# Kernel optimization log

Measured on AMD Instinct MI355X. Metric: run time of the kernel, lower is better.

Reference implementation:

```python
import jax, jax.numpy as jnp
import numpy as np

B, S, D = 2, 2048, 1024
H = 16
HD = D // H
MLP = 4096
EPS_LN = 1e-6
EPS_NORM = 1e-12
LOG_MAX = float(np.log(1.0 / 0.01))  # clamp cap for logit_scale


def setup_inputs() -> dict:
    key = jax.random.key(0)
    ks = jax.random.split(key, 12)
    sd = 0.02
    return {
        "x": jax.random.normal(ks[0], (B, S, D), jnp.float32),
        "wq": jax.random.normal(ks[1], (D, D), jnp.float32) * sd,
        "bq": jnp.zeros((D,), jnp.float32),
        "wk": jax.random.normal(ks[2], (D, D), jnp.float32) * sd,
        "bk": jnp.zeros((D,), jnp.float32),
        "wv": jax.random.normal(ks[3], (D, D), jnp.float32) * sd,
        "bv": jnp.zeros((D,), jnp.float32),
        "wo": jax.random.normal(ks[4], (D, D), jnp.float32) * sd,
        "bo": jnp.zeros((D,), jnp.float32),
        "w1": jax.random.normal(ks[5], (D, MLP), jnp.float32) * sd,
        "b1": jax.random.normal(ks[6], (MLP,), jnp.float32) * 1e-6,
        "w2": jax.random.normal(ks[7], (MLP, D), jnp.float32) * sd,
        "b2": jax.random.normal(ks[8], (D,), jnp.float32) * 1e-6,
        "ln1_g": jnp.ones((D,), jnp.float32),
        "ln1_b": jnp.zeros((D,), jnp.float32),
        "ln2_g": jnp.ones((D,), jnp.float32),
        "ln2_b": jnp.zeros((D,), jnp.float32),
        "logit_scale": jnp.log(10.0 * jnp.ones((H, 1, 1), jnp.float32)),
    }


def _layernorm(x, g, b):
    mu = jnp.mean(x, axis=-1, keepdims=True)
    var = jnp.var(x, axis=-1, keepdims=True)
    return (x - mu) * jax.lax.rsqrt(var + EPS_LN) * g + b


def _l2norm(x):
    n = jnp.linalg.norm(x, axis=-1, keepdims=True)
    return x / jnp.maximum(n, EPS_NORM)


def _split_heads(t):  # [B,S,D] -> [B,H,S,HD]
    return t.reshape(B, S, H, HD).transpose(0, 2, 1, 3)


def reference(x, wq, bq, wk, bk, wv, bv, wo, bo, w1, b1, w2, b2,
              ln1_g, ln1_b, ln2_g, ln2_b, logit_scale):
    h = x
    xn = _layernorm(x, ln1_g, ln1_b)
    q = _split_heads(xn @ wq + bq)
    k = _split_heads(xn @ wk + bk)
    v = _split_heads(xn @ wv + bv)
    # cosine attention: L2-normalize q,k, scale by clamped learnable exp temp
    scores = jnp.einsum("bhqd,bhkd->bhqk", _l2norm(q), _l2norm(k))
    scale = jnp.exp(jnp.minimum(logit_scale, LOG_MAX))  # [H,1,1]
    scores = scores * scale
    probs = jax.nn.softmax(scores, axis=-1)
    ctx = jnp.einsum("bhqk,bhkd->bhqd", probs, v)
    ctx = ctx.transpose(0, 2, 1, 3).reshape(B, S, D)
    x = ctx @ wo + bo + h
    h = x
    xn = _layernorm(x, ln2_g, ln2_b)
    y = jax.nn.gelu(xn @ w1 + b1, approximate=False) @ w2 + b2
    return y + h
```

## Files before the change

kernel.cpp:

```cpp
#include <hip/hip_runtime.h>
#include <hip/hip_bf16.h>
#include <math.h>

typedef unsigned short u16;
typedef unsigned int u32;
typedef __attribute__((ext_vector_type(8))) short bf16x8;
typedef __attribute__((ext_vector_type(4))) float f32x4;
typedef __attribute__((ext_vector_type(16))) float f32x16;

#define S_LEN 2048
#define DM 1024
#define NH 16
#define HD 64
#define MLPD 4096
#define BSZ 2
#define NROWS (BSZ * S_LEN)
#define LOGMAX 4.60517018598809f

__device__ __forceinline__ u16 f2bf(float f) {
  u32 u = __float_as_uint(f);
  u32 r = (u + 0x7fffu + ((u >> 16) & 1u)) >> 16;
  return (u16)r;
}
__device__ __forceinline__ float bf2f(u16 h) { return __uint_as_float(((u32)h) << 16); }
__device__ __forceinline__ u32 pk2(float a, float b) {
  return (u32)f2bf(a) | ((u32)f2bf(b) << 16);
}
__device__ __forceinline__ u32 cvtpk(float a, float b) {
  u32 r;
  asm("v_cvt_pk_bf16_f32 %0, %1, %2" : "=v"(r) : "v"(a), "v"(b));
  return r;
}
__device__ __forceinline__ void gld16(const void* g, void* l) {
  __builtin_amdgcn_global_load_lds(
      (const __attribute__((address_space(1))) void*)g,
      (__attribute__((address_space(3))) void*)l, 16, 0, 0);
}

__global__ __launch_bounds__(256) void ln_bf16(const float* __restrict__ x,
                                               const float* __restrict__ g,
                                               const float* __restrict__ b,
                                               u16* __restrict__ out) {
  const int row = blockIdx.x;
  const int t = threadIdx.x;
  const float* xr = x + (size_t)row * DM;
  float4 v = *reinterpret_cast<const float4*>(xr + t * 4);
  float s = v.x + v.y + v.z + v.w;
  float s2 = v.x * v.x + v.y * v.y + v.z * v.z + v.w * v.w;
#pragma unroll
  for (int off = 32; off > 0; off >>= 1) {
    s += __shfl_down(s, off);
    s2 += __shfl_down(s2, off);
  }
  __shared__ float red[8];
  __shared__ float mv[2];
  const int wid = t >> 6, lane = t & 63;
  if (lane == 0) { red[wid] = s; red[wid + 4] = s2; }
  __syncthreads();
  if (t == 0) {
    float ts = red[0] + red[1] + red[2] + red[3];
    float ts2 = red[4] + red[5] + red[6] + red[7];
    float mu = ts * (1.0f / DM);
    float var = ts2 * (1.0f / DM) - mu * mu;
    mv[0] = mu;
    mv[1] = rsqrtf(var + 1e-6f);
  }
  __syncthreads();
  const float mu = mv[0], rs = mv[1];
  float4 gv = *reinterpret_cast<const float4*>(g + t * 4);
  float4 bv = *reinterpret_cast<const float4*>(b + t * 4);
  float o0 = (v.x - mu) * rs * gv.x + bv.x;
  float o1 = (v.y - mu) * rs * gv.y + bv.y;
  float o2 = (v.z - mu) * rs * gv.z + bv.z;
  float o3 = (v.w - mu) * rs * gv.w + bv.w;
  uint2 o;
  o.x = pk2(o0, o1);
  o.y = pk2(o2, o3);
  *reinterpret_cast<uint2*>(out + (size_t)row * DM + t * 4) = o;
}

__global__ __launch_bounds__(256) void prep_weights(
    const float* __restrict__ wq, const float* __restrict__ wk, const float* __restrict__ wv,
    const float* __restrict__ wo, const float* __restrict__ w1, const float* __restrict__ w2,
    const float* __restrict__ bq, const float* __restrict__ bk, const float* __restrict__ bv,
    u16* __restrict__ wqkv_t, u16* __restrict__ wo_t, u16* __restrict__ w1_t,
    u16* __restrict__ w2_t, float* __restrict__ bqkv) {
  const int tid = threadIdx.x;
  int bid = blockIdx.x;
  if (bid < 12) {
    int i = bid * 256 + tid;
    bqkv[i] = i < 1024 ? bq[i] : (i < 2048 ? bk[i - 1024] : bv[i - 2048]);
  }
  const float* src;
  u16* dst;
  int K, N;
  if (bid < 768) {
    int m = bid >> 8;
    src = (m == 0) ? wq : (m == 1 ? wk : wv);
    dst = wqkv_t + (size_t)m * 1024 * 1024;
    K = 1024; N = 1024;
    bid &= 255;
  } else if (bid < 1024) {
    src = wo; dst = wo_t; K = 1024; N = 1024; bid -= 768;
  } else if (bid < 2048) {
    src = w1; dst = w1_t; K = 1024; N = 4096; bid -= 1024;
  } else {
    src = w2; dst = w2_t; K = 4096; N = 1024; bid -= 2048;
  }
  const int ktiles = K >> 6;
  const int k0 = (bid % ktiles) << 6, n0 = (bid / ktiles) << 6;
  __shared__ float tile[64][65];
#pragma unroll
  for (int p = 0; p < 4; ++p) {
    int r = p * 16 + (tid >> 4), c = (tid & 15) * 4;
    *reinterpret_cast<float4*>(&tile[r][c]) =
        *reinterpret_cast<const float4*>(&src[(size_t)(k0 + r) * N + n0 + c]);
  }
  __syncthreads();
#pragma unroll
  for (int p = 0; p < 4; ++p) {
    int n = p * 16 + (tid >> 4), k = (tid & 15) * 4;
    uint2 o;
    o.x = pk2(tile[k][n], tile[k + 1][n]);
    o.y = pk2(tile[k + 2][n], tile[k + 3][n]);
    *reinterpret_cast<uint2*>(&dst[(size_t)(n0 + n) * K + k0 + k]) = o;
  }
}

#define EPI_BIAS 0
#define EPI_GELU 1
#define EPI_RES 2
#define EPI_QKV 3

template <int EPI, int OUTBF>
__global__ __launch_bounds__(256) void gemm_bf16(
    const u16* __restrict__ A, const u16* __restrict__ Bt,
    const float* __restrict__ bias, const float* __restrict__ res,
    void* __restrict__ Cout, u16* __restrict__ qkx, u16* __restrict__ vtx,
    int M, int N, int K) {
  __shared__ u16 As[128 * 32];
  __shared__ u16 Bs[128 * 32];
  const int tid = threadIdx.x;
  const int wid = tid >> 6, lane = tid & 63;
  const int n0 = blockIdx.x * 128, m0 = blockIdx.y * 128;
  const int wr = wid >> 1, wc = wid & 1;

  f32x4 acc[4][4];
#pragma unroll
  for (int mi = 0; mi < 4; ++mi)
#pragma unroll
    for (int ni = 0; ni < 4; ++ni)
#pragma unroll
      for (int r = 0; r < 4; ++r) acc[mi][ni][r] = 0.0f;

  const int srow = lane >> 2;
  const int skc = (lane & 3) * 8;

  for (int k0 = 0; k0 < K; k0 += 32) {
#pragma unroll
    for (int i = 0; i < 2; ++i) {
      int c = wid * 2 + i;
      gld16(&A[(size_t)(m0 + c * 16 + srow) * K + k0 + skc], &As[c * 512]);
      gld16(&Bt[(size_t)(n0 + c * 16 + srow) * K + k0 + skc], &Bs[c * 512]);
    }
    __syncthreads();
    const int fr = lane & 15, fg = (lane >> 4) * 8;
    bf16x8 af[4], bfr[4];
#pragma unroll
    for (int mi = 0; mi < 4; ++mi)
      af[mi] = *reinterpret_cast<const bf16x8*>(&As[(wr * 64 + mi * 16 + fr) * 32 + fg]);
#pragma unroll
    for (int ni = 0; ni < 4; ++ni)
      bfr[ni] = *reinterpret_cast<const bf16x8*>(&Bs[(wc * 64 + ni * 16 + fr) * 32 + fg]);
#pragma unroll
    for (int mi = 0; mi < 4; ++mi)
#pragma unroll
      for (int ni = 0; ni < 4; ++ni)
        acc[mi][ni] =
            __builtin_amdgcn_mfma_f32_16x16x32_bf16(af[mi], bfr[ni], acc[mi][ni], 0, 0, 0);
    __syncthreads();
  }

  const int col0 = n0 + wc * 64 + (lane & 15);
  const int r4 = (lane >> 4) * 4;

  if constexpr (EPI == EPI_QKV) {
    float bias4[4];
#pragma unroll
    for (int ni = 0; ni < 4; ++ni) bias4[ni] = bias[col0 + ni * 16];
    const bool isV = (n0 + wc * 64) >= 2048;
#pragma unroll
    for (int mi = 0; mi < 4; ++mi) {
#pragma unroll
      for (int r = 0; r < 4; ++r) {
        const int row = m0 + wr * 64 + mi * 16 + r4 + r;
        float v[4];
#pragma unroll
        for (int ni = 0; ni < 4; ++ni) v[ni] = acc[mi][ni][r] + bias4[ni];
        if (!isV) {
          float ss = v[0] * v[0] + v[1] * v[1] + v[2] * v[2] + v[3] * v[3];
          ss += __shfl_xor(ss, 1);
          ss += __shfl_xor(ss, 2);
          ss += __shfl_xor(ss, 4);
          ss += __shfl_xor(ss, 8);
          float inv = 1.0f / fmaxf(sqrtf(ss), 1e-12f);
#pragma unroll
          for (int ni = 0; ni < 4; ++ni)
            qkx[(size_t)row * 2048 + col0 + ni * 16] = f2bf(v[ni] * inv);
        } else {
          const int b = row >> 11, sl = row & 2047;
#pragma unroll
          for (int ni = 0; ni < 4; ++ni) {
            const int col = col0 + ni * 16;
            const int h = (col - 2048) >> 6, d = col & 63;
            vtx[((size_t)(b * NH + h) * HD + d) * S_LEN + sl] = f2bf(v[ni]);
          }
        }
      }
    }
    return;
  }

  float bias8[4];
#pragma unroll
  for (int ni = 0; ni < 4; ++ni) bias8[ni] = bias[col0 + ni * 16];
#pragma unroll
  for (int ni = 0; ni < 4; ++ni) {
    const int col = col0 + ni * 16;
    const float bb = bias8[ni];
#pragma unroll
    for (int mi = 0; mi < 4; ++mi) {
      const int row = m0 + wr * 64 + mi * 16 + r4;
#pragma unroll
      for (int r = 0; r < 4; ++r) {
        float v = acc[mi][ni][r] + bb;
        if (EPI == EPI_GELU) v = 0.5f * v * (1.0f + erff(v * 0.70710678118654752f));
        if (EPI == EPI_RES) v += res[(size_t)(row + r) * N + col];
        if (OUTBF)
          ((u16*)Cout)[(size_t)(row + r) * N + col] = f2bf(v);
        else
          ((float*)Cout)[(size_t)(row + r) * N + col] = v;
      }
    }
  }
}

__global__ __launch_bounds__(256) void flash_mfma(const u16* __restrict__ qk,
                                                  const u16* __restrict__ vt,
                                                  const float* __restrict__ lsc,
                                                  u16* __restrict__ ctx) {
  __shared__ u16 Ks[2][64 * 72];
  __shared__ u16 Vt[2][64 * 72];
  __shared__ float den_s[128];
  const int tid = threadIdx.x;
  const int wq = tid >> 6, lane = tid & 63;
  const int lo5 = lane & 31, hi = lane >> 5;
  const int q0 = blockIdx.x * 128;
  const int bh = blockIdx.y, b = bh >> 4, h = bh & 15;
  const float scale = __expf(fminf(lsc[h], LOGMAX));

  bf16x8 qf[4];
#pragma unroll
  for (int dch = 0; dch < 4; ++dch)
    qf[dch] = *reinterpret_cast<const bf16x8*>(
        &qk[(size_t)(b * S_LEN + q0 + wq * 32 + lo5) * 2048 + h * HD + dch * 16 + hi * 8]);

  f32x16 octx[2];
#pragma unroll
  for (int dt = 0; dt < 2; ++dt)
#pragma unroll
    for (int e = 0; e < 16; ++e) octx[dt][e] = 0.0f;
  float den = 0.0f;

  const int sr = tid >> 2, sseg = tid & 3;
  const u16* kbase = qk + (size_t)(b * S_LEN + sr) * 2048 + 1024 + h * HD + sseg * 8;
  const u16* vbase = vt + (size_t)(bh * HD + sr) * S_LEN + sseg * 8;

  {
    uint4 k0 = *reinterpret_cast<const uint4*>(kbase);
    uint4 k1 = *reinterpret_cast<const uint4*>(kbase + 32);
    uint4 v0 = *reinterpret_cast<const uint4*>(vbase);
    uint4 v1 = *reinterpret_cast<const uint4*>(vbase + 32);
    *reinterpret_cast<uint4*>(&Ks[0][sr * 72 + sseg * 8]) = k0;
    *reinterpret_cast<uint4*>(&Ks[0][sr * 72 + 32 + sseg * 8]) = k1;
    *reinterpret_cast<uint4*>(&Vt[0][sr * 72 + sseg * 8]) = v0;
    *reinterpret_cast<uint4*>(&Vt[0][sr * 72 + 32 + sseg * 8]) = v1;
  }
  __syncthreads();

  int buf = 0;
  for (int kt = 0; kt < S_LEN / 64; ++kt) {
    const int nx = (kt + 1) & (S_LEN / 64 - 1);
    uint4 k0 = *reinterpret_cast<const uint4*>(kbase + (size_t)nx * 64 * 2048);
    uint4 k1 = *reinterpret_cast<const uint4*>(kbase + (size_t)nx * 64 * 2048 + 32);
    uint4 v0 = *reinterpret_cast<const uint4*>(vbase + nx * 64);
    uint4 v1 = *reinterpret_cast<const uint4*>(vbase + nx * 64 + 32);

    const u16* Kc = &Ks[buf][0];
    const u16* Vc = &Vt[buf][0];

    f32x16 sc[2];
#pragma unroll
    for (int ktile = 0; ktile < 2; ++ktile)
#pragma unroll
      for (int e = 0; e < 16; ++e) sc[ktile][e] = 0.0f;
#pragma unroll
    for (int ktile = 0; ktile < 2; ++ktile)
#pragma unroll
      for (int dch = 0; dch < 4; ++dch) {
        bf16x8 kf = *reinterpret_cast<const bf16x8*>(
            &Kc[(ktile * 32 + lo5) * 72 + dch * 16 + hi * 8]);
        sc[ktile] = __builtin_amdgcn_mfma_f32_32x32x16_bf16(kf, qf[dch], sc[ktile], 0, 0, 0);
      }

    u32 pk[2][8];
    float ps = 0.0f;
#pragma unroll
    for (int ktile = 0; ktile < 2; ++ktile) {
      float p[16];
#pragma unroll
      for (int r = 0; r < 16; ++r) {
        p[r] = __expf(fmaf(scale, sc[ktile][r], -scale));
        ps += p[r];
      }
#pragma unroll
      for (int n = 0; n < 4; ++n) {
        pk[ktile][n * 2] = cvtpk(p[n * 4], p[n * 4 + 1]);
        pk[ktile][n * 2 + 1] = cvtpk(p[n * 4 + 2], p[n * 4 + 3]);
      }
    }
    ps += __shfl_xor(ps, 32);
    den += ps;

#pragma unroll
    for (int ktile = 0; ktile < 2; ++ktile)
#pragma unroll
      for (int cc = 0; cc < 2; ++cc) {
        u32 o0 = pk[ktile][(2 * cc) * 2], o1 = pk[ktile][(2 * cc) * 2 + 1];
        u32 e0 = pk[ktile][(2 * cc + 1) * 2], e1 = pk[ktile][(2 * cc + 1) * 2 + 1];
        u32 s0 = (u32)__shfl_xor((int)o0, 32);
        u32 s1 = (u32)__shfl_xor((int)o1, 32);
        u32 t0 = (u32)__shfl_xor((int)e0, 32);
        u32 t1 = (u32)__shfl_xor((int)e1, 32);
        union { u32 u[4]; bf16x8 v; } pf;
        pf.u[0] = hi ? t0 : o0;
        pf.u[1] = hi ? t1 : o1;
        pf.u[2] = hi ? e0 : s0;
        pf.u[3] = hi ? e1 : s1;
        const int kvo = (ktile * 2 + cc) * 16 + hi * 8;
#pragma unroll
        for (int dt = 0; dt < 2; ++dt) {
          bf16x8 vf = *reinterpret_cast<const bf16x8*>(&Vc[(dt * 32 + lo5) * 72 + kvo]);
          octx[dt] = __builtin_amdgcn_mfma_f32_32x32x16_bf16(pf.v, vf, octx[dt], 0, 0, 0);
        }
      }

    *reinterpret_cast<uint4*>(&Ks[buf ^ 1][sr * 72 + sseg * 8]) = k0;
    *reinterpret_cast<uint4*>(&Ks[buf ^ 1][sr * 72 + 32 + sseg * 8]) = k1;
    *reinterpret_cast<uint4*>(&Vt[buf ^ 1][sr * 72 + sseg * 8]) = v0;
    *reinterpret_cast<uint4*>(&Vt[buf ^ 1][sr * 72 + 32 + sseg * 8]) = v1;
    __syncthreads();
    buf ^= 1;
  }

  if (hi == 0) den_s[wq * 32 + lo5] = den;
  __syncthreads();
#pragma unroll
  for (int r = 0; r < 16; ++r) {
    const int ql = (r & 3) + 8 * (r >> 2) + 4 * hi;
    const float inv = 1.0f / den_s[wq * 32 + ql];
    const size_t row = (size_t)(b * S_LEN + q0 + wq * 32 + ql);
#pragma unroll
    for (int dt = 0; dt < 2; ++dt)
      ctx[row * DM + h * HD + dt * 32 + lo5] = f2bf(octx[dt][r] * inv);
  }
}

extern "C" void kernel_launch(void* const* d_in, const int* in_sizes, int n_in,
                              void* d_out, int out_size, void* d_ws, size_t ws_size,
                              hipStream_t stream) {
  const float* x    = (const float*)d_in[0];
  const float* wq   = (const float*)d_in[1];
  const float* bq   = (const float*)d_in[2];
  const float* wk   = (const float*)d_in[3];
  const float* bk   = (const float*)d_in[4];
  const float* wv   = (const float*)d_in[5];
  const float* bv   = (const float*)d_in[6];
  const float* wo   = (const float*)d_in[7];
  const float* bo   = (const float*)d_in[8];
  const float* w1   = (const float*)d_in[9];
  const float* b1   = (const float*)d_in[10];
  const float* w2   = (const float*)d_in[11];
  const float* b2   = (const float*)d_in[12];
  const float* ln1g = (const float*)d_in[13];
  const float* ln1b = (const float*)d_in[14];
  const float* ln2g = (const float*)d_in[15];
  const float* ln2b = (const float*)d_in[16];
  const float* lsc  = (const float*)d_in[17];

  char* ws = (char*)d_ws;
  u16* wqkv_t = (u16*)(ws + 0);
  u16* wo_t   = (u16*)(ws + 6291456);
  u16* w1_t   = (u16*)(ws + 8388608);
  u16* w2_t   = (u16*)(ws + 16777216);
  float* bqkv = (float*)(ws + 25165824);
  u16* xn     = (u16*)(ws + 25178112);
  float* x2   = (float*)(ws + 33566720);
  u16* qkbuf  = (u16*)(ws + 50343936);
  u16* vtbuf  = (u16*)(ws + 67121152);
  u16* ctx    = (u16*)(ws + 75509760);
  u16* h1     = qkbuf;

  prep_weights<<<dim3(3072), dim3(256), 0, stream>>>(wq, wk, wv, wo, w1, w2, bq, bk, bv,
                                                     wqkv_t, wo_t, w1_t, w2_t, bqkv);
  ln_bf16<<<dim3(NROWS), dim3(256), 0, stream>>>(x, ln1g, ln1b, xn);
  gemm_bf16<EPI_QKV, 1><<<dim3(3072 / 128, NROWS / 128), dim3(256), 0, stream>>>(
      xn, wqkv_t, bqkv, nullptr, nullptr, qkbuf, vtbuf, NROWS, 3072, 1024);
  flash_mfma<<<dim3(S_LEN / 128, BSZ * NH), dim3(256), 0, stream>>>(qkbuf, vtbuf, lsc, ctx);
  gemm_bf16<EPI_RES, 0><<<dim3(1024 / 128, NROWS / 128), dim3(256), 0, stream>>>(
      ctx, wo_t, bo, x, x2, nullptr, nullptr, NROWS, 1024, 1024);
  ln_bf16<<<dim3(NROWS), dim3(256), 0, stream>>>(x2, ln2g, ln2b, xn);
  gemm_bf16<EPI_GELU, 1><<<dim3(4096 / 128, NROWS / 128), dim3(256), 0, stream>>>(
      xn, w1_t, b1, nullptr, h1, nullptr, nullptr, NROWS, 4096, 1024);
  gemm_bf16<EPI_RES, 0><<<dim3(1024 / 128, NROWS / 128), dim3(256), 0, stream>>>(
      h1, w2_t, b2, x2, (float*)d_out, nullptr, nullptr, NROWS, 1024, 4096);
}
```

Baseline: 441.9 us.

## Double-buffer GEMM shared-memory tiles to overlap global loads with MFMA

Splits the A and B LDS tiles into two buffers. The next K-slice is issued with gld16 into the other buffer before the MFMAs run on the current one, which drops one __syncthreads per iteration. The intent is to hide global-load latency behind matrix math. The cost is doubled LDS use, which may lower occupancy. Whether the loads really overlap depends on how gld16 waits (for example on vmcnt) before the barrier.

```diff
diff --git a/kernel.cpp b/kernel.cpp
--- a/kernel.cpp
+++ b/kernel.cpp
@@ -138,8 +138,8 @@
     const float* __restrict__ bias, const float* __restrict__ res,
     void* __restrict__ Cout, u16* __restrict__ qkx, u16* __restrict__ vtx,
     int M, int N, int K) {
-  __shared__ u16 As[128 * 32];
-  __shared__ u16 Bs[128 * 32];
+  __shared__ u16 As[2][128 * 32];
+  __shared__ u16 Bs[2][128 * 32];
   const int tid = threadIdx.x;
   const int wid = tid >> 6, lane = tid & 63;
   const int n0 = blockIdx.x * 128, m0 = blockIdx.y * 128;
@@ -155,23 +155,35 @@
 
   const int srow = lane >> 2;
   const int skc = (lane & 3) * 8;
-
+  const int c0 = wid * 2, c1 = wid * 2 + 1;
+  const u16* ab0 = A + (size_t)(m0 + c0 * 16 + srow) * K + skc;
+  const u16* ab1 = A + (size_t)(m0 + c1 * 16 + srow) * K + skc;
+  const u16* bb0 = Bt + (size_t)(n0 + c0 * 16 + srow) * K + skc;
+  const u16* bb1 = Bt + (size_t)(n0 + c1 * 16 + srow) * K + skc;
+
+  gld16(ab0, &As[0][c0 * 512]);
+  gld16(ab1, &As[0][c1 * 512]);
+  gld16(bb0, &Bs[0][c0 * 512]);
+  gld16(bb1, &Bs[0][c1 * 512]);
+  __syncthreads();
+
+  const int fr = lane & 15, fg = (lane >> 4) * 8;
+  int cur = 0;
   for (int k0 = 0; k0 < K; k0 += 32) {
-#pragma unroll
-    for (int i = 0; i < 2; ++i) {
-      int c = wid * 2 + i;
-      gld16(&A[(size_t)(m0 + c * 16 + srow) * K + k0 + skc], &As[c * 512]);
-      gld16(&Bt[(size_t)(n0 + c * 16 + srow) * K + k0 + skc], &Bs[c * 512]);
+    if (k0 + 32 < K) {
+      const int nxt = cur ^ 1;
+      gld16(ab0 + k0 + 32, &As[nxt][c0 * 512]);
+      gld16(ab1 + k0 + 32, &As[nxt][c1 * 512]);
+      gld16(bb0 + k0 + 32, &Bs[nxt][c0 * 512]);
+      gld16(bb1 + k0 + 32, &Bs[nxt][c1 * 512]);
     }
-    __syncthreads();
-    const int fr = lane & 15, fg = (lane >> 4) * 8;
     bf16x8 af[4], bfr[4];
 #pragma unroll
     for (int mi = 0; mi < 4; ++mi)
-      af[mi] = *reinterpret_cast<const bf16x8*>(&As[(wr * 64 + mi * 16 + fr) * 32 + fg]);
+      af[mi] = *reinterpret_cast<const bf16x8*>(&As[cur][(wr * 64 + mi * 16 + fr) * 32 + fg]);
 #pragma unroll
     for (int ni = 0; ni < 4; ++ni)
-      bfr[ni] = *reinterpret_cast<const bf16x8*>(&Bs[(wc * 64 + ni * 16 + fr) * 32 + fg]);
+      bfr[ni] = *reinterpret_cast<const bf16x8*>(&Bs[cur][(wc * 64 + ni * 16 + fr) * 32 + fg]);
 #pragma unroll
     for (int mi = 0; mi < 4; ++mi)
 #pragma unroll
@@ -179,6 +191,7 @@
         acc[mi][ni] =
             __builtin_amdgcn_mfma_f32_16x16x32_bf16(af[mi], bfr[ni], acc[mi][ni], 0, 0, 0);
     __syncthreads();
+    cur ^= 1;
   }
 
   const int col0 = n0 + wc * 64 + (lane & 15);
```

After: 422.3 us. -4.4%, faster.
